# Kernel tuning notes

Measured on AMD Instinct MI355X. Metric: run time of the kernel, lower is better.

The kernel has to match this reference:

```python
import jax, jax.numpy as jnp
import numpy as np

N, E, D_IN, HID, D_OUT = 200000, 5000000, 128, 16, 2


def setup_inputs() -> dict:
    key = jax.random.key(0)
    ks = jax.random.split(key, 8)
    x = jax.random.normal(ks[0], (N, D_IN), dtype=jnp.float32)
    edge_index = jax.random.randint(ks[1], (2, E), 0, N, dtype=jnp.int32)
    W1 = jax.random.normal(ks[2], (D_IN, HID), dtype=jnp.float32) / np.sqrt(D_IN)
    b1 = jnp.zeros((HID,), dtype=jnp.float32)
    W3 = jax.random.normal(ks[3], (HID, HID), dtype=jnp.float32) / np.sqrt(HID)
    b3 = jnp.zeros((HID,), dtype=jnp.float32)
    W2 = jax.random.normal(ks[4], (HID, D_OUT), dtype=jnp.float32) / np.sqrt(HID)
    b2 = jnp.zeros((D_OUT,), dtype=jnp.float32)
    return {"x": x, "edge_index": edge_index, "W1": W1, "b1": b1,
            "W3": W3, "b3": b3, "W2": W2, "b2": b2}


def reference(x, edge_index, W1, b1, W3, b3, W2, b2):
    # GCNConv: add self-loops, symmetric normalization, aggregate, linear+bias.
    src, dst = edge_index[0], edge_index[1]
    loops = jnp.arange(N, dtype=src.dtype)
    src_f = jnp.concatenate([src, loops])  # [E+N]
    dst_f = jnp.concatenate([dst, loops])
    deg = jax.ops.segment_sum(jnp.ones_like(src_f, dtype=jnp.float32), dst_f,
                              num_segments=N)
    dis = jnp.where(deg > 0, jax.lax.rsqrt(jnp.maximum(deg, 1.0)), 0.0)
    norm = dis[src_f] * dis[dst_f]  # [E+N]

    def gcn_conv(h, W, b):
        h = h @ W                                   # [N, F_out] small GEMM
        msg = h[src_f] * norm[:, None]              # gather + scale
        agg = jax.ops.segment_sum(msg, dst_f, num_segments=N)  # scatter-add
        return agg + b

    h = jax.nn.relu(gcn_conv(x, W1, b1))    # conv1 (dropout is identity in eval)
    h = jax.nn.relu(gcn_conv(h, W3, b3))    # conv3 loop (conv_number-2 = 1 iter)
    h = gcn_conv(h, W2, b2)                 # conv2
    return jax.nn.log_softmax(h, axis=1)
```

## Files before the change

kernel.cpp:

```cpp
#include <hip/hip_runtime.h>

#define NN 200000
#define NE 5000000
#define DIN 128
#define HID 16
#define DOUT 2
#define BSZ 391
#define NB 512
#define LBITS 9
#define NCH 4
#define SLICE_DIV 50000
#define NK (NB * NCH)
#define NKB 512
#define SKEYS 2048
#define PB 512
#define PT 512

static_assert((size_t)NB * BSZ >= NN, "bucket coverage");
static_assert((NN - 1) / SLICE_DIV == NCH - 1, "slice count");
static_assert(NE % 4 == 0, "int4 edge reads");


__global__ __launch_bounds__(PT) void hist_pass(const int4* __restrict__ dst4,
                                                int* __restrict__ blockHist) {
    __shared__ int h[NKB];
    for (int k = threadIdx.x; k < NKB; k += PT) h[k] = 0;
    __syncthreads();
    const int NI = NE / 4;
    for (int i = blockIdx.x * PT + threadIdx.x; i < NI; i += PB * PT) {
        int4 d = dst4[i];
        atomicAdd(&h[d.x / BSZ], 1);
        atomicAdd(&h[d.y / BSZ], 1);
        atomicAdd(&h[d.z / BSZ], 1);
        atomicAdd(&h[d.w / BSZ], 1);
    }
    __syncthreads();
    for (int k = threadIdx.x; k < NKB; k += PT)
        blockHist[(size_t)blockIdx.x * NKB + k] = h[k];
}

__global__ __launch_bounds__(256) void tot_pass(const int* __restrict__ blockHist,
                                                int* __restrict__ chunkStart) {
    int k = blockIdx.x * 256 + threadIdx.x;
    if (k >= NKB) return;
    int s = 0;
#pragma unroll 16
    for (int b = 0; b < PB; ++b) s += blockHist[(size_t)b * NKB + k];
    chunkStart[k] = s;
}

__global__ __launch_bounds__(NKB) void scan_keys(int* __restrict__ chunkStart) {
    __shared__ int wsum[8];
    int t = threadIdx.x;
    int lane = t & 63, w = t >> 6;
    int v = chunkStart[t];
    int inc = v;
    for (int off = 1; off < 64; off <<= 1) {
        int nb = __shfl_up(inc, off, 64);
        if (lane >= off) inc += nb;
    }
    if (lane == 63) wsum[w] = inc;
    __syncthreads();
    if (t == 0) {
        int car = 0;
#pragma unroll
        for (int i = 0; i < 8; ++i) { int u = wsum[i]; wsum[i] = car; car += u; }
    }
    __syncthreads();
    chunkStart[t] = inc - v + wsum[w];
    if (t == 0) chunkStart[NKB] = NE;
}

__global__ __launch_bounds__(256) void offsets_pass(int* __restrict__ blockHist,
                                                    const int* __restrict__ chunkStart) {
    int k = blockIdx.x * 256 + threadIdx.x;
    if (k >= NKB) return;
    int r = chunkStart[k];
#pragma unroll 8
    for (int b = 0; b < PB; ++b) {
        size_t idx = (size_t)b * NKB + k;
        int v = blockHist[idx];
        blockHist[idx] = r;
        r += v;
    }
}

__global__ __launch_bounds__(PT) void scatter_pass(const int4* __restrict__ src4,
                                                   const int4* __restrict__ dst4,
                                                   const int* __restrict__ blockHist,
                                                   unsigned* __restrict__ pedge) {
    __shared__ int cur[NKB];
    for (int k = threadIdx.x; k < NKB; k += PT)
        cur[k] = blockHist[(size_t)blockIdx.x * NKB + k];
    __syncthreads();
    const int NI = NE / 4;
    for (int i = blockIdx.x * PT + threadIdx.x; i < NI; i += PB * PT) {
        int4 s = src4[i];
        int4 d = dst4[i];
        int b0 = d.x / BSZ, b1 = d.y / BSZ, b2 = d.z / BSZ, b3 = d.w / BSZ;
        int p0 = atomicAdd(&cur[b0], 1);
        int p1 = atomicAdd(&cur[b1], 1);
        int p2 = atomicAdd(&cur[b2], 1);
        int p3 = atomicAdd(&cur[b3], 1);
        pedge[p0] = ((unsigned)s.x << LBITS) | (unsigned)(d.x - b0 * BSZ);
        pedge[p1] = ((unsigned)s.y << LBITS) | (unsigned)(d.y - b1 * BSZ);
        pedge[p2] = ((unsigned)s.z << LBITS) | (unsigned)(d.z - b2 * BSZ);
        pedge[p3] = ((unsigned)s.w << LBITS) | (unsigned)(d.w - b3 * BSZ);
    }
}


__global__ __launch_bounds__(512) void subsort(const unsigned* __restrict__ pedge,
                                               const int* __restrict__ chunkStart,
                                               int* __restrict__ pedge2,
                                               int* __restrict__ rowStart,
                                               float* __restrict__ dis) {
    __shared__ int h[SKEYS];
    __shared__ int wsum[8];
    int t = threadIdx.x;
    int b = blockIdx.x;
    int lane = t & 63, w = t >> 6;
    int e0 = chunkStart[b], e1 = chunkStart[b + 1];
    for (int k = t; k < SKEYS; k += 512) h[k] = 0;
    __syncthreads();
    for (int i = e0 + t; i < e1; i += 512) {
        unsigned p = pedge[i];
        int sv = (int)(p >> LBITS);
        atomicAdd(&h[(sv / SLICE_DIV) * 512 + (p & 511u)], 1);
    }
    __syncthreads();
    if (t < BSZ) {
        int dg = 1;
#pragma unroll
        for (int s = 0; s < NCH; ++s) dg += h[s * 512 + t];
        int node = b * BSZ + t;
        if (node < NN) dis[node] = rsqrtf((float)dg);
    }
    int vals[4];
    int s = 0;
#pragma unroll
    for (int j = 0; j < 4; ++j) { vals[j] = h[t * 4 + j]; s += vals[j]; }
    int inc = s;
    for (int off = 1; off < 64; off <<= 1) {
        int nb = __shfl_up(inc, off, 64);
        if (lane >= off) inc += nb;
    }
    if (lane == 63) wsum[w] = inc;
    __syncthreads();
    if (t == 0) {
        int car = 0;
#pragma unroll
        for (int i = 0; i < 8; ++i) { int u = wsum[i]; wsum[i] = car; car += u; }
    }
    __syncthreads();
    int run = inc - s + wsum[w];
#pragma unroll
    for (int j = 0; j < 4; ++j) {
        int k = t * 4 + j;
        h[k] = run;
        int dl = k & 511, sl = k >> 9;
        if (dl < BSZ)
            rowStart[(size_t)(b * NCH + sl) * BSZ + dl] = e0 + run;
        run += vals[j];
    }
    __syncthreads();
    for (int i = e0 + t; i < e1; i += 512) {
        unsigned p = pedge[i];
        int sv = (int)(p >> LBITS);
        int key = (sv / SLICE_DIV) * 512 + (p & 511u);
        int pos = atomicAdd(&h[key], 1);
        pedge2[e0 + pos] = sv;
    }
    if (b == 0 && t == 0) rowStart[(size_t)NK * BSZ] = NE;
}


#define GXT 512
#define GXR 128
__global__ __launch_bounds__(GXT) void gemm_x_w1(const float* __restrict__ x,
                                                 const float* __restrict__ W,
                                                 const float* __restrict__ dis,
                                                 float* __restrict__ out) {
    __shared__ float w[DIN * HID];
    int t = threadIdx.x;
    for (int i = t; i < DIN * HID; i += GXT) w[i] = W[i];
    __syncthreads();
    int row = blockIdx.x * GXR + (t >> 2);
    int c0 = (t & 3) * 4;
    if (row >= NN) return;
    const float4* xr = reinterpret_cast<const float4*>(x + (size_t)row * DIN);
    float ax = 0.f, ay = 0.f, az = 0.f, aw = 0.f;
#pragma unroll
    for (int k4 = 0; k4 < DIN / 4; ++k4) {
        float4 xv = xr[k4];
        float4 w0 = *reinterpret_cast<const float4*>(&w[(4 * k4 + 0) * HID + c0]);
        float4 w1 = *reinterpret_cast<const float4*>(&w[(4 * k4 + 1) * HID + c0]);
        float4 w2 = *reinterpret_cast<const float4*>(&w[(4 * k4 + 2) * HID + c0]);
        float4 w3 = *reinterpret_cast<const float4*>(&w[(4 * k4 + 3) * HID + c0]);
        ax += xv.x * w0.x + xv.y * w1.x + xv.z * w2.x + xv.w * w3.x;
        ay += xv.x * w0.y + xv.y * w1.y + xv.z * w2.y + xv.w * w3.y;
        az += xv.x * w0.z + xv.y * w1.z + xv.z * w2.z + xv.w * w3.z;
        aw += xv.x * w0.w + xv.y * w1.w + xv.z * w2.w + xv.w * w3.w;
    }
    float dd = dis[row];
    *reinterpret_cast<float4*>(&out[(size_t)row * HID + c0]) =
        make_float4(ax * dd, ay * dd, az * dd, aw * dd);
}

__global__ __launch_bounds__(256) void gemm_h_w16(const float* __restrict__ h,
                                                  const float* __restrict__ W,
                                                  const float* __restrict__ dis,
                                                  float* __restrict__ out) {
    __shared__ float w[HID * HID];
    if (threadIdx.x < HID * HID) w[threadIdx.x] = W[threadIdx.x];
    __syncthreads();
    int row = blockIdx.x * 16 + (threadIdx.x >> 4);
    int c = threadIdx.x & 15;
    if (row >= NN) return;
    const float4* hr = reinterpret_cast<const float4*>(h + (size_t)row * HID);
    float acc = 0.f;
#pragma unroll
    for (int k4 = 0; k4 < HID / 4; ++k4) {
        float4 v = hr[k4];
        acc += v.x * w[(4 * k4 + 0) * HID + c] + v.y * w[(4 * k4 + 1) * HID + c]
             + v.z * w[(4 * k4 + 2) * HID + c] + v.w * w[(4 * k4 + 3) * HID + c];
    }
    out[row * HID + c] = acc * dis[row];
}

__global__ __launch_bounds__(256) void gemm_h_w2(const float* __restrict__ h,
                                                 const float* __restrict__ W,
                                                 const float* __restrict__ dis,
                                                 float* __restrict__ out) {
    int t = blockIdx.x * 256 + threadIdx.x;
    int row = t >> 1;
    int c = t & 1;
    if (row >= NN) return;
    const float* hr = h + (size_t)row * HID;
    float acc = 0.f;
#pragma unroll
    for (int k = 0; k < HID; ++k) acc += hr[k] * W[k * DOUT + c];
    out[row * DOUT + c] = acc * dis[row];
}


__device__ __forceinline__ void acc_edges(const int* __restrict__ pedge2,
                                          const float4* __restrict__ xs4,
                                          int e, int e1, int c4, float4& a) {
    for (; e + 3 < e1; e += 4) {
        int s0 = pedge2[e], s1 = pedge2[e + 1];
        int s2 = pedge2[e + 2], s3 = pedge2[e + 3];
        float4 u0 = xs4[(s0 << 2) + c4];
        float4 u1 = xs4[(s1 << 2) + c4];
        float4 u2 = xs4[(s2 << 2) + c4];
        float4 u3 = xs4[(s3 << 2) + c4];
        a.x += (u0.x + u1.x) + (u2.x + u3.x);
        a.y += (u0.y + u1.y) + (u2.y + u3.y);
        a.z += (u0.z + u1.z) + (u2.z + u3.z);
        a.w += (u0.w + u1.w) + (u2.w + u3.w);
    }
    for (; e < e1; ++e) {
        float4 u = xs4[(pedge2[e] << 2) + c4];
        a.x += u.x; a.y += u.y; a.z += u.z; a.w += u.w;
    }
}

__global__ __launch_bounds__(1024, 8) void agg16_all(const int* __restrict__ pedge2,
                                                     const int* __restrict__ rowStart,
                                                     const float* __restrict__ xs,
                                                     const float* __restrict__ dis,
                                                     const float* __restrict__ bias,
                                                     float* __restrict__ buf,
                                                     int relu) {
    int t = threadIdx.x;
    int b = blockIdx.x;
    int base = b * BSZ;
    int c4 = t & 3;
    int q = t >> 2;
    int g0 = (q * BSZ) >> 8;
    int g1 = ((q + 1) * BSZ) >> 8;
    bool two = (g1 - g0) == 2;
    int n0 = base + g0, n1 = base + g0 + 1;
    bool v0 = n0 < NN;
    bool v1 = two && (n1 < NN);
    const float4* xs4 = reinterpret_cast<const float4*>(xs);
    float4* buf4 = reinterpret_cast<float4*>(buf);
    int sA[NCH], sB[NCH], sC[NCH];
#pragma unroll
    for (int r = 0; r < NCH; ++r) {
        const int* rs = rowStart + (size_t)(b * NCH + r) * BSZ + g0;
        sA[r] = v0 ? rs[0] : 0;
        sB[r] = v0 ? rs[1] : 0;
        sC[r] = v1 ? rs[2] : 0;
    }
    float4 a0 = make_float4(0.f, 0.f, 0.f, 0.f);
    float4 a1 = a0;
    if (v0) a0 = xs4[(n0 << 2) + c4];
    if (v1) a1 = xs4[(n1 << 2) + c4];
#pragma unroll
    for (int r = 0; r < NCH; ++r) {
        if (v0) acc_edges(pedge2, xs4, sA[r], sB[r], c4, a0);
        if (v1) acc_edges(pedge2, xs4, sB[r], sC[r], c4, a1);
    }
    float4 bb = reinterpret_cast<const float4*>(bias)[c4];
    if (v0) {
        float dd = dis[n0];
        float4 v = make_float4(dd * a0.x + bb.x, dd * a0.y + bb.y,
                               dd * a0.z + bb.z, dd * a0.w + bb.w);
        if (relu) { v.x = fmaxf(v.x, 0.f); v.y = fmaxf(v.y, 0.f);
                    v.z = fmaxf(v.z, 0.f); v.w = fmaxf(v.w, 0.f); }
        buf4[(n0 << 2) + c4] = v;
    }
    if (v1) {
        float dd = dis[n1];
        float4 v = make_float4(dd * a1.x + bb.x, dd * a1.y + bb.y,
                               dd * a1.z + bb.z, dd * a1.w + bb.w);
        if (relu) { v.x = fmaxf(v.x, 0.f); v.y = fmaxf(v.y, 0.f);
                    v.z = fmaxf(v.z, 0.f); v.w = fmaxf(v.w, 0.f); }
        buf4[(n1 << 2) + c4] = v;
    }
}

__global__ __launch_bounds__(512) void agg2_lsm(const int* __restrict__ pedge2,
                                                const int* __restrict__ rowStart,
                                                const float* __restrict__ xs,
                                                const float* __restrict__ dis,
                                                const float* __restrict__ bias,
                                                float* __restrict__ out) {
    int t = threadIdx.x;
    int b = blockIdx.x;
    if (t >= BSZ) return;
    int node = b * BSZ + t;
    if (node >= NN) return;
    const float2* xs2 = reinterpret_cast<const float2*>(xs);
    float a0 = 0.f, a1 = 0.f;
#pragma unroll
    for (int s = 0; s < NCH; ++s) {
        const int* rs = rowStart + (size_t)(b * NCH + s) * BSZ;
        int e = rs[t], e1 = rs[t + 1];
        for (; e + 3 < e1; e += 4) {
            int s0 = pedge2[e], s1 = pedge2[e + 1];
            int s2 = pedge2[e + 2], s3 = pedge2[e + 3];
            float2 v0 = xs2[s0], v1 = xs2[s1], v2 = xs2[s2], v3 = xs2[s3];
            a0 += (v0.x + v1.x) + (v2.x + v3.x);
            a1 += (v0.y + v1.y) + (v2.y + v3.y);
        }
        for (; e < e1; ++e) {
            float2 v = xs2[pedge2[e]];
            a0 += v.x; a1 += v.y;
        }
    }
    float2 sv = xs2[node];
    float d = dis[node];
    float v0 = (a0 + sv.x) * d + bias[0];
    float v1 = (a1 + sv.y) * d + bias[1];
    float m = fmaxf(v0, v1);
    float lse = m + logf(__expf(v0 - m) + __expf(v1 - m));
    reinterpret_cast<float2*>(out)[node] = make_float2(v0 - lse, v1 - lse);
}


extern "C" void kernel_launch(void* const* d_in, const int* in_sizes, int n_in,
                              void* d_out, int out_size, void* d_ws, size_t ws_size,
                              hipStream_t stream) {
    const float* x = (const float*)d_in[0];
    const int* ei = (const int*)d_in[1];
    const float* W1 = (const float*)d_in[2];
    const float* b1 = (const float*)d_in[3];
    const float* W3 = (const float*)d_in[4];
    const float* b3 = (const float*)d_in[5];
    const float* W2 = (const float*)d_in[6];
    const float* b2 = (const float*)d_in[7];
    float* out = (float*)d_out;

    const int4* src4 = (const int4*)ei;
    const int4* dst4 = (const int4*)(ei + NE);

    int* W = (int*)d_ws;
    unsigned* pedge = (unsigned*)W;
    int* pedge2 = W + NE;
    int* rowStart = W + 2 * (size_t)NE;
    int* blockHist = rowStart + (size_t)NK * BSZ + 4;
    int* chunkStart = blockHist + (size_t)PB * NKB;
    float* dis = (float*)(chunkStart + NKB + 4);
    float* bufB = dis + NN;
    float* bufA = (float*)W;

    const int B = 256;
    auto cdiv = [](long long a, long long b) { return (int)((a + b - 1) / b); };

    hist_pass<<<PB, PT, 0, stream>>>(dst4, blockHist);
    tot_pass<<<cdiv(NKB, 256), 256, 0, stream>>>(blockHist, chunkStart);
    scan_keys<<<1, NKB, 0, stream>>>(chunkStart);
    offsets_pass<<<cdiv(NKB, 256), 256, 0, stream>>>(blockHist, chunkStart);
    scatter_pass<<<PB, PT, 0, stream>>>(src4, dst4, blockHist, pedge);
    subsort<<<NB, 512, 0, stream>>>(pedge, chunkStart, pedge2, rowStart, dis);

    gemm_x_w1<<<cdiv(NN, GXR), GXT, 0, stream>>>(x, W1, dis, bufA);
    agg16_all<<<NB, 1024, 0, stream>>>(pedge2, rowStart, bufA, dis, b1, bufB, 1);

    gemm_h_w16<<<cdiv(NN, 16), B, 0, stream>>>(bufB, W3, dis, bufA);
    agg16_all<<<NB, 1024, 0, stream>>>(pedge2, rowStart, bufA, dis, b3, bufB, 1);

    gemm_h_w2<<<cdiv((long long)NN * DOUT, B), B, 0, stream>>>(bufB, W2, dis, bufA);
    agg2_lsm<<<NB, 512, 0, stream>>>(pedge2, rowStart, bufA, dis, b2, out);
}
```

Baseline: 283.1 us.

## Cache subsort edges in LDS, widen edge loads, interleave two-node gathers

```diff
diff --git a/kernel.cpp b/kernel.cpp
--- a/kernel.cpp
+++ b/kernel.cpp
@@ -15,10 +15,11 @@
 #define SKEYS 2048
 #define PB 512
 #define PT 512
+#define ECAP 9216
 
 static_assert((size_t)NB * BSZ >= NN, "bucket coverage");
 static_assert((NN - 1) / SLICE_DIV == NCH - 1, "slice count");
-static_assert(NE % 4 == 0, "int4 edge reads");
+static_assert(NE % 8 == 0, "int4-pair edge reads");
 
 
 __global__ __launch_bounds__(PT) void hist_pass(const int4* __restrict__ dst4,
@@ -26,13 +27,18 @@
     __shared__ int h[NKB];
     for (int k = threadIdx.x; k < NKB; k += PT) h[k] = 0;
     __syncthreads();
-    const int NI = NE / 4;
-    for (int i = blockIdx.x * PT + threadIdx.x; i < NI; i += PB * PT) {
-        int4 d = dst4[i];
-        atomicAdd(&h[d.x / BSZ], 1);
-        atomicAdd(&h[d.y / BSZ], 1);
-        atomicAdd(&h[d.z / BSZ], 1);
-        atomicAdd(&h[d.w / BSZ], 1);
+    const int NI8 = NE / 8;
+    for (int j = blockIdx.x * PT + threadIdx.x; j < NI8; j += PB * PT) {
+        int4 d0 = dst4[2 * j];
+        int4 d1 = dst4[2 * j + 1];
+        atomicAdd(&h[d0.x / BSZ], 1);
+        atomicAdd(&h[d0.y / BSZ], 1);
+        atomicAdd(&h[d0.z / BSZ], 1);
+        atomicAdd(&h[d0.w / BSZ], 1);
+        atomicAdd(&h[d1.x / BSZ], 1);
+        atomicAdd(&h[d1.y / BSZ], 1);
+        atomicAdd(&h[d1.z / BSZ], 1);
+        atomicAdd(&h[d1.w / BSZ], 1);
     }
     __syncthreads();
     for (int k = threadIdx.x; k < NKB; k += PT)
@@ -93,19 +99,30 @@
     for (int k = threadIdx.x; k < NKB; k += PT)
         cur[k] = blockHist[(size_t)blockIdx.x * NKB + k];
     __syncthreads();
-    const int NI = NE / 4;
-    for (int i = blockIdx.x * PT + threadIdx.x; i < NI; i += PB * PT) {
-        int4 s = src4[i];
-        int4 d = dst4[i];
-        int b0 = d.x / BSZ, b1 = d.y / BSZ, b2 = d.z / BSZ, b3 = d.w / BSZ;
+    const int NI8 = NE / 8;
+    for (int j = blockIdx.x * PT + threadIdx.x; j < NI8; j += PB * PT) {
+        int4 s0 = src4[2 * j];
+        int4 s1 = src4[2 * j + 1];
+        int4 d0 = dst4[2 * j];
+        int4 d1 = dst4[2 * j + 1];
+        int b0 = d0.x / BSZ, b1 = d0.y / BSZ, b2 = d0.z / BSZ, b3 = d0.w / BSZ;
+        int b4 = d1.x / BSZ, b5 = d1.y / BSZ, b6 = d1.z / BSZ, b7 = d1.w / BSZ;
         int p0 = atomicAdd(&cur[b0], 1);
         int p1 = atomicAdd(&cur[b1], 1);
         int p2 = atomicAdd(&cur[b2], 1);
         int p3 = atomicAdd(&cur[b3], 1);
-        pedge[p0] = ((unsigned)s.x << LBITS) | (unsigned)(d.x - b0 * BSZ);
-        pedge[p1] = ((unsigned)s.y << LBITS) | (unsigned)(d.y - b1 * BSZ);
-        pedge[p2] = ((unsigned)s.z << LBITS) | (unsigned)(d.z - b2 * BSZ);
-        pedge[p3] = ((unsigned)s.w << LBITS) | (unsigned)(d.w - b3 * BSZ);
+        int p4 = atomicAdd(&cur[b4], 1);
+        int p5 = atomicAdd(&cur[b5], 1);
+        int p6 = atomicAdd(&cur[b6], 1);
+        int p7 = atomicAdd(&cur[b7], 1);
+        pedge[p0] = ((unsigned)s0.x << LBITS) | (unsigned)(d0.x - b0 * BSZ);
+        pedge[p1] = ((unsigned)s0.y << LBITS) | (unsigned)(d0.y - b1 * BSZ);
+        pedge[p2] = ((unsigned)s0.z << LBITS) | (unsigned)(d0.z - b2 * BSZ);
+        pedge[p3] = ((unsigned)s0.w << LBITS) | (unsigned)(d0.w - b3 * BSZ);
+        pedge[p4] = ((unsigned)s1.x << LBITS) | (unsigned)(d1.x - b4 * BSZ);
+        pedge[p5] = ((unsigned)s1.y << LBITS) | (unsigned)(d1.y - b5 * BSZ);
+        pedge[p6] = ((unsigned)s1.z << LBITS) | (unsigned)(d1.z - b6 * BSZ);
+        pedge[p7] = ((unsigned)s1.w << LBITS) | (unsigned)(d1.w - b7 * BSZ);
     }
 }
 
@@ -116,15 +133,18 @@
                                                int* __restrict__ rowStart,
                                                float* __restrict__ dis) {
     __shared__ int h[SKEYS];
+    __shared__ unsigned ebuf[ECAP];
     __shared__ int wsum[8];
     int t = threadIdx.x;
     int b = blockIdx.x;
     int lane = t & 63, w = t >> 6;
     int e0 = chunkStart[b], e1 = chunkStart[b + 1];
+    int n = e1 - e0;
     for (int k = t; k < SKEYS; k += 512) h[k] = 0;
     __syncthreads();
-    for (int i = e0 + t; i < e1; i += 512) {
-        unsigned p = pedge[i];
+    for (int i = t; i < n; i += 512) {
+        unsigned p = pedge[e0 + i];
+        if (i < ECAP) ebuf[i] = p;
         int sv = (int)(p >> LBITS);
         atomicAdd(&h[(sv / SLICE_DIV) * 512 + (p & 511u)], 1);
     }
@@ -164,8 +184,8 @@
         run += vals[j];
     }
     __syncthreads();
-    for (int i = e0 + t; i < e1; i += 512) {
-        unsigned p = pedge[i];
+    for (int i = t; i < n; i += 512) {
+        unsigned p = (i < ECAP) ? ebuf[i] : pedge[e0 + i];
         int sv = (int)(p >> LBITS);
         int key = (sv / SLICE_DIV) * 512 + (p & 511u);
         int pos = atomicAdd(&h[key], 1);
@@ -263,6 +283,36 @@
         float4 u = xs4[(pedge2[e] << 2) + c4];
         a.x += u.x; a.y += u.y; a.z += u.z; a.w += u.w;
     }
+}
+
+__device__ __forceinline__ void acc2(const int* __restrict__ pedge2,
+                                     const float4* __restrict__ xs4,
+                                     int eA, int eAe, int eB, int eBe,
+                                     int c4, float4& a0, float4& a1) {
+    while (eA + 3 < eAe && eB + 3 < eBe) {
+        int i0 = pedge2[eA], i1 = pedge2[eA + 1], i2 = pedge2[eA + 2], i3 = pedge2[eA + 3];
+        int j0 = pedge2[eB], j1 = pedge2[eB + 1], j2 = pedge2[eB + 2], j3 = pedge2[eB + 3];
+        float4 uA0 = xs4[(i0 << 2) + c4];
+        float4 uA1 = xs4[(i1 << 2) + c4];
+        float4 uA2 = xs4[(i2 << 2) + c4];
+        float4 uA3 = xs4[(i3 << 2) + c4];
+        float4 uB0 = xs4[(j0 << 2) + c4];
+        float4 uB1 = xs4[(j1 << 2) + c4];
+        float4 uB2 = xs4[(j2 << 2) + c4];
+        float4 uB3 = xs4[(j3 << 2) + c4];
+        a0.x += (uA0.x + uA1.x) + (uA2.x + uA3.x);
+        a0.y += (uA0.y + uA1.y) + (uA2.y + uA3.y);
+        a0.z += (uA0.z + uA1.z) + (uA2.z + uA3.z);
+        a0.w += (uA0.w + uA1.w) + (uA2.w + uA3.w);
+        a1.x += (uB0.x + uB1.x) + (uB2.x + uB3.x);
+        a1.y += (uB0.y + uB1.y) + (uB2.y + uB3.y);
+        a1.z += (uB0.z + uB1.z) + (uB2.z + uB3.z);
+        a1.w += (uB0.w + uB1.w) + (uB2.w + uB3.w);
+        eA += 4;
+        eB += 4;
+    }
+    acc_edges(pedge2, xs4, eA, eAe, c4, a0);
+    acc_edges(pedge2, xs4, eB, eBe, c4, a1);
 }
 
 __global__ __launch_bounds__(1024, 8) void agg16_all(const int* __restrict__ pedge2,
@@ -299,8 +349,8 @@
     if (v1) a1 = xs4[(n1 << 2) + c4];
 #pragma unroll
     for (int r = 0; r < NCH; ++r) {
-        if (v0) acc_edges(pedge2, xs4, sA[r], sB[r], c4, a0);
-        if (v1) acc_edges(pedge2, xs4, sB[r], sC[r], c4, a1);
+        if (v1) acc2(pedge2, xs4, sA[r], sB[r], sB[r], sC[r], c4, a0, a1);
+        else if (v0) acc_edges(pedge2, xs4, sA[r], sB[r], c4, a0);
     }
     float4 bb = reinterpret_cast<const float4*>(bias)[c4];
     if (v0) {
```

Result: slower. 306.3 us (+8.2%).
